# Optimization experiments

Measured on AMD Instinct MI355X. Metric: run time of the kernel, lower is better.

Reference implementation:

```python
import jax, jax.numpy as jnp
import numpy as np

L, H, NH, HD, FF, S, B, V, NL = 2, 2048, 16, 128, 4096, 1024, 2, 32000, 4
R, SCALING, BLK = 2, 16.0 / 2.0, 64  # LoRA r=2, alpha=16 -> scaling 8; NF4 blocksize 64
NF4 = jnp.array([-1.0, -0.6961928009986877, -0.5250730514526367, -0.39491748809814453,
                 -0.28444138169288635, -0.18477343022823334, -0.09105003625154495, 0.0,
                 0.07958029955625534, 0.16093020141124725, 0.24611230194568634,
                 0.33791524171829224, 0.44070982933044434, 0.5626170039176941,
                 0.7229568362236023, 1.0], dtype=jnp.float32)

def dequant(codes, scales):
    # codes [out, in] int -> NF4 values; scales [out, in//BLK] absmax per 64-block
    return NF4[codes] * jnp.repeat(scales, BLK, axis=-1)

def qlin(x, codes, scales, A, Bm):
    # fused dequant + GEMM + LoRA low-rank update: x @ (Wd + s*B@A).T
    W = dequant(codes, scales)
    return x @ W.T + SCALING * ((x @ A.T) @ Bm.T)

def layer_norm(x, g, b):
    mu = jnp.mean(x, -1, keepdims=True)
    var = jnp.var(x, -1, keepdims=True)
    return (x - mu) * jax.lax.rsqrt(var + 1e-5) * g + b

def rope(x):  # x [B,S,NH,HD]
    half = HD // 2
    inv = 1.0 / (10000.0 ** (jnp.arange(half, dtype=jnp.float32) / half))
    ang = jnp.arange(S, dtype=jnp.float32)[:, None] * inv[None, :]
    cos = jnp.concatenate([jnp.cos(ang)] * 2, -1)[None, :, None, :]
    sin = jnp.concatenate([jnp.sin(ang)] * 2, -1)[None, :, None, :]
    x1, x2 = x[..., :half], x[..., half:]
    return x * cos + jnp.concatenate([-x2, x1], -1) * sin

def setup_inputs() -> dict:
    key = jax.random.key(0)
    it = iter(jax.random.split(key, 64))
    nrm = lambda shp, s: jax.random.normal(next(it), shp, jnp.float32) * s
    cod = lambda shp: jax.random.randint(next(it), shp, 0, 16, jnp.int32)
    scl = lambda shp: jax.random.uniform(next(it), shp, jnp.float32) * 0.02 + 1e-3
    lens = jax.random.randint(next(it), (B,), S // 2, S + 1)
    return dict(
        input_ids=jax.random.randint(next(it), (B, S), 0, V, jnp.int32),
        attention_mask=(jnp.arange(S)[None, :] < lens[:, None]).astype(jnp.int32),
        labels=jax.random.randint(next(it), (B,), 0, NL, jnp.int32),
        embed=nrm((V, H), 0.02),
        qkv_codes=cod((L, 3 * H, H)), qkv_scales=scl((L, 3 * H, H // BLK)),
        qkv_A=nrm((L, R, H), 0.01), qkv_B=nrm((L, 3 * H, R), 0.01),
        dense_codes=cod((L, H, H)), dense_scales=scl((L, H, H // BLK)),
        dense_A=nrm((L, R, H), 0.01), dense_B=nrm((L, H, R), 0.01),
        min_codes=cod((L, 2 * FF, H)), min_scales=scl((L, 2 * FF, H // BLK)),
        min_A=nrm((L, R, H), 0.01), min_B=nrm((L, 2 * FF, R), 0.01),
        mout_codes=cod((L, H, FF)), mout_scales=scl((L, H, FF // BLK)),
        mout_A=nrm((L, R, FF), 0.01), mout_B=nrm((L, H, R), 0.01),
        ln1_g=jnp.ones((L, H)), ln1_b=jnp.zeros((L, H)),
        ln2_g=jnp.ones((L, H)), ln2_b=jnp.zeros((L, H)),
        lnf_g=jnp.ones((H,)), lnf_b=jnp.zeros((H,)),
        classifier_w=nrm((NL, H), 0.01),
    )

def reference(input_ids, attention_mask, labels, embed, qkv_codes, qkv_scales, qkv_A, qkv_B,
              dense_codes, dense_scales, dense_A, dense_B, min_codes, min_scales, min_A, min_B,
              mout_codes, mout_scales, mout_A, mout_B, ln1_g, ln1_b, ln2_g, ln2_b,
              lnf_g, lnf_b, classifier_w):
    x = embed[input_ids]  # [B,S,H]
    mask = jnp.tril(jnp.ones((S, S), bool))[None, None] & (attention_mask[:, None, None, :] > 0)
    for l in range(L):
        h = layer_norm(x, ln1_g[l], ln1_b[l])
        qkv = qlin(h, qkv_codes[l], qkv_scales[l], qkv_A[l], qkv_B[l]).reshape(B, S, NH, 3 * HD)
        q, k, v = qkv[..., :HD], qkv[..., HD:2 * HD], qkv[..., 2 * HD:]
        q, k = rope(q), rope(k)
        scores = jnp.einsum('bqhd,bkhd->bhqk', q, k) / np.float32(np.sqrt(HD))
        probs = jax.nn.softmax(jnp.where(mask, scores, jnp.float32(-1e30)), -1)
        attn = jnp.einsum('bhqk,bkhd->bqhd', probs, v).reshape(B, S, H)
        x = x + qlin(attn, dense_codes[l], dense_scales[l], dense_A[l], dense_B[l])
        h2 = layer_norm(x, ln2_g[l], ln2_b[l])
        u = qlin(h2, min_codes[l], min_scales[l], min_A[l], min_B[l])  # [B,S,2*FF] packed SwiGLU
        g = jax.nn.silu(u[..., :FF]) * u[..., FF:]
        x = x + qlin(g, mout_codes[l], mout_scales[l], mout_A[l], mout_B[l])
    x = layer_norm(x, lnf_g, lnf_b)
    eos = x[jnp.arange(B), attention_mask.sum(1) - 1]  # last non-padded token hidden
    logits = eos @ classifier_w.T
    logp = jax.nn.log_softmax(logits, -1)
    loss = -jnp.mean(logp[jnp.arange(B), labels])
    return loss, logits
```

## Files before the change

### kernel.cpp

```cpp
#include <hip/hip_runtime.h>

typedef unsigned short u16;
typedef __attribute__((ext_vector_type(4))) float f32x4;
typedef __attribute__((ext_vector_type(8))) short short8;
typedef __attribute__((ext_vector_type(4))) short short4v;

constexpr int CL  = 2;
constexpr int CH  = 2048;
constexpr int CNH = 16;
constexpr int CHD = 128;
constexpr int CFF = 4096;
constexpr int CS  = 1024;
constexpr int CB  = 2;
constexpr int CNL = 4;
constexpr int CM  = CB * CS;
#define SCALING 8.0f

__device__ __constant__ float NF4TAB[16] = {
    -1.0f, -0.6961928009986877f, -0.5250730514526367f, -0.39491748809814453f,
    -0.28444138169288635f, -0.18477343022823334f, -0.09105003625154495f, 0.0f,
    0.07958029955625534f, 0.16093020141124725f, 0.24611230194568634f,
    0.33791524171829224f, 0.44070982933044434f, 0.5626170039176941f,
    0.7229568362236023f, 1.0f};

__device__ __forceinline__ u16 f2bf(float f) {
  union { float f; unsigned u; } v; v.f = f;
  unsigned r = v.u + 0x7fffu + ((v.u >> 16) & 1u);
  return (u16)(r >> 16);
}
__device__ __forceinline__ float bf2f(u16 u) {
  union { unsigned u; float f; } v; v.u = ((unsigned)u) << 16;
  return v.f;
}

template <int N> __device__ __forceinline__ void wait_vm() {
  if constexpr (N == 0)      asm volatile("s_waitcnt vmcnt(0)" ::: "memory");
  else if constexpr (N == 6) asm volatile("s_waitcnt vmcnt(6)" ::: "memory");
  else if constexpr (N == 8) asm volatile("s_waitcnt vmcnt(8)" ::: "memory");
  else                       asm volatile("s_waitcnt vmcnt(0)" ::: "memory");
}

__device__ __forceinline__ float blockReduceSum(float v) {
  __shared__ float sh[4];
  #pragma unroll
  for (int o = 32; o > 0; o >>= 1) v += __shfl_down(v, o);
  __syncthreads();
  if ((threadIdx.x & 63) == 0) sh[threadIdx.x >> 6] = v;
  __syncthreads();
  return sh[0] + sh[1] + sh[2] + sh[3];
}

__global__ void k_embed(const int* __restrict__ ids, const float* __restrict__ emb,
                        float* __restrict__ x) {
  int m = blockIdx.x;
  const float4* src = (const float4*)(emb + (size_t)ids[m] * CH);
  float4* dst = (float4*)(x + (size_t)m * CH);
  for (int i = threadIdx.x; i < CH / 4; i += 256) dst[i] = src[i];
}

__global__ void k_ln_xa(const float* __restrict__ x, const float* __restrict__ g,
                        const float* __restrict__ b, const float* __restrict__ A,
                        u16* __restrict__ o, float* __restrict__ xA) {
  int m = blockIdx.x, tid = threadIdx.x;
  const float* row = x + (size_t)m * CH;
  float s = 0.f, s2 = 0.f;
  for (int i = tid; i < CH / 4; i += 256) {
    float4 v = ((const float4*)row)[i];
    s += v.x + v.y + v.z + v.w;
    s2 += v.x * v.x + v.y * v.y + v.z * v.z + v.w * v.w;
  }
  s = blockReduceSum(s);
  s2 = blockReduceSum(s2);
  float mu = s / CH, var = s2 / CH - mu * mu;
  float rs = rsqrtf(var + 1e-5f);
  u16* orow = o + (size_t)m * CH;
  float s0 = 0.f, s1 = 0.f;
  for (int i = tid; i < CH / 4; i += 256) {
    float4 v = ((const float4*)row)[i];
    float4 gv = ((const float4*)g)[i];
    float4 bv = ((const float4*)b)[i];
    float4 a0 = ((const float4*)A)[i];
    float4 a1 = ((const float4*)(A + CH))[i];
    float h0 = (v.x - mu) * rs * gv.x + bv.x;
    float h1 = (v.y - mu) * rs * gv.y + bv.y;
    float h2 = (v.z - mu) * rs * gv.z + bv.z;
    float h3 = (v.w - mu) * rs * gv.w + bv.w;
    short4v ov = { (short)f2bf(h0), (short)f2bf(h1), (short)f2bf(h2), (short)f2bf(h3) };
    *(short4v*)(orow + i * 4) = ov;
    s0 += h0 * a0.x + h1 * a0.y + h2 * a0.z + h3 * a0.w;
    s1 += h0 * a1.x + h1 * a1.y + h2 * a1.z + h3 * a1.w;
  }
  s0 = blockReduceSum(s0);
  s1 = blockReduceSum(s1);
  if (tid == 0) { xA[2 * m] = s0; xA[2 * m + 1] = s1; }
}

__global__ void k_xa(const u16* __restrict__ xb, const float* __restrict__ A,
                     float* __restrict__ xA, int K) {
  int m = blockIdx.x, tid = threadIdx.x;
  const u16* row = xb + (size_t)m * K;
  float s0 = 0.f, s1 = 0.f;
  for (int c = tid; c < K / 8; c += 256) {
    short8 v = *(const short8*)(row + c * 8);
    #pragma unroll
    for (int e = 0; e < 8; ++e) {
      float f = bf2f((u16)v[e]);
      s0 += f * A[c * 8 + e];
      s1 += f * A[K + c * 8 + e];
    }
  }
  s0 = blockReduceSum(s0);
  s1 = blockReduceSum(s1);
  if (tid == 0) { xA[2 * m] = s0; xA[2 * m + 1] = s1; }
}

__global__ void k_dequant(const int* __restrict__ codes, const float* __restrict__ scales,
                          u16* __restrict__ w, int kshift, long total) {
  __shared__ float lut[16];
  if (threadIdx.x < 16) lut[threadIdx.x] = NF4TAB[threadIdx.x];
  __syncthreads();
  long base = ((long)blockIdx.x * 256 + threadIdx.x) * 8;
  if (base >= total) return;
  long n = base >> kshift;
  int k = (int)(base & ((1L << kshift) - 1));
  float sc = scales[(size_t)n * (1 << (kshift - 6)) + (k >> 6)];
  const int* cp = codes + base;
  short8 o;
  #pragma unroll
  for (int i = 0; i < 8; ++i) o[i] = (short)f2bf(lut[cp[i] & 15] * sc);
  *(short8*)(w + base) = o;
}

__global__ void k_ropetab(float* __restrict__ cosT, float* __restrict__ sinT) {
  int i = blockIdx.x * 256 + threadIdx.x;
  if (i >= CS * 64) return;
  int s = i >> 6, d = i & 63;
  float inv = powf(10000.0f, -(float)d / 64.0f);
  float a = (float)s * inv;
  cosT[i] = cosf(a);
  sinT[i] = sinf(a);
}

__global__ void k_rope(const u16* __restrict__ qkv, const float* __restrict__ cosT,
                       const float* __restrict__ sinT, u16* __restrict__ Qb,
                       u16* __restrict__ Kb) {
  int bid = blockIdx.x;
  int s = bid & (CS - 1);
  int z = bid >> 10;
  int b = z >> 4, h = z & 15;
  int d = threadIdx.x;
  const u16* base = qkv + ((size_t)(b * CS + s)) * (3 * CH) + h * (3 * CHD);
  int dh = d & 63;
  float c = cosT[s * 64 + dh], sn = sinT[s * 64 + dh];
  float sgn = (d < 64) ? -1.0f : 1.0f;
  float q = bf2f(base[d]),       qp = bf2f(base[d ^ 64]);
  float k = bf2f(base[CHD + d]), kp = bf2f(base[CHD + (d ^ 64)]);
  size_t oi = ((size_t)z * CS + s) * CHD + d;
  Qb[oi] = f2bf(q * c + sgn * qp * sn);
  Kb[oi] = f2bf(k * c + sgn * kp * sn);
}

__global__ void k_vtrans(const u16* __restrict__ qkv, u16* __restrict__ Vt) {
  __shared__ u16 tile[32][33];
  int z = blockIdx.z;
  int b = z >> 4, h = z & 15;
  int s0 = blockIdx.x * 32, d0 = blockIdx.y * 32;
  int tx = threadIdx.x, ty = threadIdx.y;
  #pragma unroll
  for (int i = 0; i < 32; i += 8)
    tile[ty + i][tx] =
        qkv[((size_t)(b * CS + s0 + ty + i)) * (3 * CH) + h * (3 * CHD) + 2 * CHD + d0 + tx];
  __syncthreads();
  #pragma unroll
  for (int i = 0; i < 32; i += 8)
    Vt[((size_t)z * CHD + d0 + ty + i) * CS + s0 + tx] = tile[tx][ty + i];
}

__global__ __launch_bounds__(256, 2) void k_flash(
    const u16* __restrict__ Qb, const u16* __restrict__ Kb, const u16* __restrict__ Vt,
    const int* __restrict__ amask, u16* __restrict__ out) {
  __shared__ u16 Ks[64 * 128];
  __shared__ u16 Vs[128 * 64];
  __shared__ float bias[CS];
  __shared__ u16 Ps[4][16][80];
  int bid = blockIdx.x;
  int qt = 15 - (bid >> 5);
  int z = bid & 31;
  int b = z >> 4, h = z & 15;
  int tid = threadIdx.x, lane = tid & 63, wid = tid >> 6;
  int lrow = lane & 15, lgrp = lane >> 4;
  const u16* Qz = Qb + (size_t)z * CS * CHD;
  const u16* Kz = Kb + (size_t)z * CS * CHD;
  const u16* Vz = Vt + (size_t)z * CHD * CS;

  for (int i = tid; i < CS; i += 256)
    bias[i] = amask[b * CS + i] ? 0.f : -1e30f;

  int qrow = qt * 64 + wid * 16 + lrow;
  short8 qf[4];
  #pragma unroll
  for (int kk = 0; kk < 4; ++kk)
    qf[kk] = *(const short8*)(Qz + (size_t)qrow * CHD + kk * 32 + lgrp * 8);

  float m_r[4], l_r[4];
  #pragma unroll
  for (int r = 0; r < 4; ++r) { m_r[r] = -3e38f; l_r[r] = 0.f; }
  f32x4 o_acc[8];
  #pragma unroll
  for (int dj = 0; dj < 8; ++dj) o_acc[dj] = (f32x4){0.f, 0.f, 0.f, 0.f};

  const float SCL = 0.08838834764831845f;

  for (int t = 0; t <= qt; ++t) {
    int k0 = t * 64;
    __syncthreads();
    #pragma unroll
    for (int it = 0; it < 4; ++it) {
      int c = it * 256 + tid;
      int key = c >> 4, ch = c & 15;
      short8 v = *(const short8*)(Kz + (size_t)(k0 + key) * CHD + ch * 8);
      *(short8*)((char*)Ks + key * 256 + ((ch * 16) ^ ((key & 7) << 4))) = v;
    }
    #pragma unroll
    for (int it = 0; it < 4; ++it) {
      int c = it * 256 + tid;
      int d = c >> 3, ch = c & 7;
      short8 v = *(const short8*)(Vz + (size_t)d * CS + k0 + ch * 8);
      *(short8*)((char*)Vs + d * 128 + ((ch * 16) ^ ((d & 7) << 4))) = v;
    }
    __syncthreads();

    f32x4 s_acc[4];
    #pragma unroll
    for (int nj = 0; nj < 4; ++nj) s_acc[nj] = (f32x4){0.f, 0.f, 0.f, 0.f};
    #pragma unroll
    for (int kk = 0; kk < 4; ++kk) {
      #pragma unroll
      for (int nj = 0; nj < 4; ++nj) {
        int key = nj * 16 + lrow;
        short8 kf = *(const short8*)((const char*)Ks + key * 256 +
                                     (((kk * 32 + lgrp * 8) * 2) ^ ((key & 7) << 4)));
        s_acc[nj] = __builtin_amdgcn_mfma_f32_16x16x32_bf16(qf[kk], kf, s_acc[nj], 0, 0, 0);
      }
    }

    bool diag = (t == qt);
    float p[4][4], mx[4];
    #pragma unroll
    for (int r = 0; r < 4; ++r) {
      int ql = wid * 16 + 4 * lgrp + r;
      float rm = -3e38f;
      #pragma unroll
      for (int nj = 0; nj < 4; ++nj) {
        int kl = nj * 16 + lrow;
        float v = s_acc[nj][r] * SCL + bias[k0 + kl];
        if (diag && kl > ql) v = -1e30f;
        p[nj][r] = v;
        rm = fmaxf(rm, v);
      }
      mx[r] = rm;
    }
    #pragma unroll
    for (int o = 1; o < 16; o <<= 1)
      #pragma unroll
      for (int r = 0; r < 4; ++r) mx[r] = fmaxf(mx[r], __shfl_xor(mx[r], o));
    float ps[4], alpha[4];
    #pragma unroll
    for (int r = 0; r < 4; ++r) {
      float mn = fmaxf(m_r[r], mx[r]);
      alpha[r] = __expf(m_r[r] - mn);
      m_r[r] = mn;
      float acc = 0.f;
      #pragma unroll
      for (int nj = 0; nj < 4; ++nj) {
        float e = __expf(p[nj][r] - mn);
        p[nj][r] = e;
        acc += e;
      }
      ps[r] = acc;
    }
    #pragma unroll
    for (int o = 1; o < 16; o <<= 1)
      #pragma unroll
      for (int r = 0; r < 4; ++r) ps[r] += __shfl_xor(ps[r], o);
    #pragma unroll
    for (int r = 0; r < 4; ++r) {
      l_r[r] = l_r[r] * alpha[r] + ps[r];
      #pragma unroll
      for (int dj = 0; dj < 8; ++dj) o_acc[dj][r] *= alpha[r];
    }

    #pragma unroll
    for (int r = 0; r < 4; ++r)
      #pragma unroll
      for (int nj = 0; nj < 4; ++nj)
        Ps[wid][4 * lgrp + r][nj * 16 + lrow] = f2bf(p[nj][r]);
    #pragma unroll
    for (int kk2 = 0; kk2 < 2; ++kk2) {
      short8 pa = *(const short8*)(&Ps[wid][lrow][kk2 * 32 + lgrp * 8]);
      #pragma unroll
      for (int dj = 0; dj < 8; ++dj) {
        int d = dj * 16 + lrow;
        short8 vf = *(const short8*)((const char*)Vs + d * 128 +
                                     (((kk2 * 32 + lgrp * 8) * 2) ^ ((d & 7) << 4)));
        o_acc[dj] = __builtin_amdgcn_mfma_f32_16x16x32_bf16(pa, vf, o_acc[dj], 0, 0, 0);
      }
    }
  }

  #pragma unroll
  for (int r = 0; r < 4; ++r) {
    float inv = 1.0f / l_r[r];
    int qg = qt * 64 + wid * 16 + 4 * lgrp + r;
    size_t rowoff = ((size_t)(b * CS + qg)) * CH + h * CHD;
    #pragma unroll
    for (int dj = 0; dj < 8; ++dj)
      out[rowoff + dj * 16 + lrow] = f2bf(o_acc[dj][r] * inv);
  }
}

__global__ void k_silu_xa(const u16* __restrict__ u, const float* __restrict__ A,
                          u16* __restrict__ g, float* __restrict__ xA) {
  int m = blockIdx.x, tid = threadIdx.x;
  const u16* urow = u + (size_t)m * (2 * CFF);
  u16* grow = g + (size_t)m * CFF;
  float s0 = 0.f, s1 = 0.f;
  for (int c = tid; c < CFF / 8; c += 256) {
    short8 va = *(const short8*)(urow + c * 8);
    short8 vb = *(const short8*)(urow + CFF + c * 8);
    short8 og;
    #pragma unroll
    for (int e = 0; e < 8; ++e) {
      float a = bf2f((u16)va[e]);
      float bb = bf2f((u16)vb[e]);
      float gg = (a / (1.0f + __expf(-a))) * bb;
      og[e] = (short)f2bf(gg);
      s0 += gg * A[c * 8 + e];
      s1 += gg * A[CFF + c * 8 + e];
    }
    *(short8*)(grow + c * 8) = og;
  }
  s0 = blockReduceSum(s0);
  s1 = blockReduceSum(s1);
  if (tid == 0) { xA[2 * m] = s0; xA[2 * m + 1] = s1; }
}

template <int BM, int BN, int TW, int WM, int WN, int OUT_BF16, int LORA, int RESID>
__global__ __launch_bounds__(TW, 2) void k_gemm3(
    const u16* __restrict__ Ag, const u16* __restrict__ Bg, void* __restrict__ Cout,
    const float* __restrict__ resid, const float* __restrict__ xA,
    const float* __restrict__ lB, int K, int N) {
  constexpr int WROWS = BM / WM, WCOLS = BN / WN;
  constexpr int M_REP = WROWS / 16, N_REP = WCOLS / 16;
  constexpr int LA = BM * 8 / TW, LBN = BN * 8 / TW;
  constexpr int LPT = LA + LBN;
  __shared__ __align__(16) u16 As[2][BM * 64];
  __shared__ __align__(16) u16 Bs[2][BN * 64];
  int tid = threadIdx.x, lane = tid & 63, wid = tid >> 6;
  int wm = wid / WN, wn = wid % WN;
  int gx = gridDim.x, nwg = gx * gridDim.y;
  int bid = blockIdx.y * gx + blockIdx.x;
  int qq = nwg >> 3, rr = nwg & 7;
  int xcd = bid & 7, lid = bid >> 3;
  int swz = (xcd < rr ? xcd * (qq + 1) : rr * (qq + 1) + (xcd - rr) * qq) + lid;
  long bm = (long)(swz % gx) * BM, bn = (long)(swz / gx) * BN;

  f32x4 acc[M_REP][N_REP];
  #pragma unroll
  for (int i = 0; i < M_REP; ++i)
    #pragma unroll
    for (int j = 0; j < N_REP; ++j) acc[i][j] = (f32x4){0.f, 0.f, 0.f, 0.f};

  auto stage = [&](int buf, int t) {
    int k0 = t * 64;
    #pragma unroll
    for (int i = 0; i < LA; ++i) {
      int f = i * TW + tid;
      int r = f >> 3, g = (f & 7) ^ (r & 7);
      __builtin_amdgcn_global_load_lds(
          (const __attribute__((address_space(1))) void*)(Ag + (size_t)(bm + r) * K + k0 + g * 8),
          (__attribute__((address_space(3))) void*)(&As[buf][f * 8]), 16, 0, 0);
    }
    #pragma unroll
    for (int i = 0; i < LBN; ++i) {
      int f = i * TW + tid;
      int r = f >> 3, g = (f & 7) ^ (r & 7);
      __builtin_amdgcn_global_load_lds(
          (const __attribute__((address_space(1))) void*)(Bg + (size_t)(bn + r) * K + k0 + g * 8),
          (__attribute__((address_space(3))) void*)(&Bs[buf][f * 8]), 16, 0, 0);
    }
  };

  int NT = K >> 6;
  stage(0, 0);
  stage(1, 1);

  int kg = lane >> 4, lr = lane & 15;
  for (int t = 0; t < NT; ++t) {
    int buf = t & 1;
    if (t + 1 < NT) wait_vm<LPT>();
    else            wait_vm<0>();
    __builtin_amdgcn_s_barrier();

    short8 af[2][M_REP], bfr[2][N_REP];
    #pragma unroll
    for (int kk = 0; kk < 2; ++kk) {
      int au = kk * 4 + kg;
      #pragma unroll
      for (int i = 0; i < M_REP; ++i) {
        int r = wm * WROWS + i * 16 + lr;
        af[kk][i] = *(const short8*)(&As[buf][r * 64 + ((au ^ (r & 7)) << 3)]);
      }
      #pragma unroll
      for (int j = 0; j < N_REP; ++j) {
        int r = wn * WCOLS + j * 16 + lr;
        bfr[kk][j] = *(const short8*)(&Bs[buf][r * 64 + ((au ^ (r & 7)) << 3)]);
      }
    }
    asm volatile("s_waitcnt lgkmcnt(0)" ::: "memory");
    __builtin_amdgcn_s_barrier();
    if (t + 2 < NT) stage(buf, t + 2);

    __builtin_amdgcn_s_setprio(1);
    #pragma unroll
    for (int kk = 0; kk < 2; ++kk)
      #pragma unroll
      for (int i = 0; i < M_REP; ++i)
        #pragma unroll
        for (int j = 0; j < N_REP; ++j)
          acc[i][j] = __builtin_amdgcn_mfma_f32_16x16x32_bf16(af[kk][i], bfr[kk][j], acc[i][j], 0, 0, 0);
    __builtin_amdgcn_s_setprio(0);
  }

  #pragma unroll
  for (int i = 0; i < M_REP; ++i) {
    #pragma unroll
    for (int r = 0; r < 4; ++r) {
      long m = bm + wm * WROWS + i * 16 + ((lane >> 4) << 2) + r;
      float xa0 = 0.f, xa1 = 0.f;
      if (LORA) { xa0 = xA[2 * m]; xa1 = xA[2 * m + 1]; }
      #pragma unroll
      for (int j = 0; j < N_REP; ++j) {
        long n = bn + wn * WCOLS + j * 16 + (lane & 15);
        float v = acc[i][j][r];
        if (LORA) v += SCALING * (xa0 * lB[2 * n] + xa1 * lB[2 * n + 1]);
        if (RESID) v += resid[m * N + n];
        if (OUT_BF16)
          ((u16*)Cout)[m * N + n] = f2bf(v);
        else
          ((float*)Cout)[m * N + n] = v;
      }
    }
  }
}

__global__ void k_final(const float* __restrict__ x, const int* __restrict__ amask,
                        const int* __restrict__ labels, const float* __restrict__ g,
                        const float* __restrict__ bb, const float* __restrict__ cw,
                        float* __restrict__ out) {
  __shared__ float xr[CH];
  __shared__ float lg[CB][CNL];
  int tid = threadIdx.x;
  for (int b = 0; b < CB; ++b) {
    float fc = 0.f;
    for (int k = tid; k < CS; k += 256) fc += (amask[b * CS + k] != 0) ? 1.0f : 0.0f;
    int len = (int)(blockReduceSum(fc) + 0.5f);
    const float* row = x + ((size_t)b * CS + (len - 1)) * CH;
    float s = 0.f, s2 = 0.f;
    for (int k = tid; k < CH; k += 256) { float v = row[k]; s += v; s2 += v * v; }
    s = blockReduceSum(s);
    s2 = blockReduceSum(s2);
    float mu = s / CH, var = s2 / CH - mu * mu;
    float rs = rsqrtf(var + 1e-5f);
    for (int k = tid; k < CH; k += 256) xr[k] = (row[k] - mu) * rs * g[k] + bb[k];
    __syncthreads();
    for (int c = 0; c < CNL; ++c) {
      float p = 0.f;
      for (int k = tid; k < CH; k += 256) p += xr[k] * cw[c * CH + k];
      p = blockReduceSum(p);
      if (tid == 0) { lg[b][c] = p; out[1 + b * CNL + c] = p; }
    }
    __syncthreads();
  }
  if (tid == 0) {
    float loss = 0.f;
    for (int b = 0; b < CB; ++b) {
      float mx = -1e30f;
      for (int c = 0; c < CNL; ++c) mx = fmaxf(mx, lg[b][c]);
      float se = 0.f;
      for (int c = 0; c < CNL; ++c) se += expf(lg[b][c] - mx);
      float lse = mx + logf(se);
      loss -= (lg[b][labels[b]] - lse);
    }
    out[0] = loss / CB;
  }
}

static constexpr size_t X_OFF  = 0;
static constexpr size_t H_OFF  = X_OFF + (size_t)CM * CH * 4;
static constexpr size_t W_OFF  = H_OFF + (size_t)CM * CH * 2;
static constexpr size_t SC_OFF = W_OFF + (size_t)8192 * 2048 * 2;
static constexpr size_t PR_OFF = SC_OFF + (size_t)32 * CS * CS * 4;
static constexpr size_t XA_OFF = PR_OFF + (size_t)32 * CS * CS * 2;
static constexpr size_t CS_OFF = XA_OFF + (size_t)CM * 2 * 4;
static constexpr size_t SN_OFF = CS_OFF + (size_t)CS * 64 * 4;
static constexpr size_t WS_END = SN_OFF + (size_t)CS * 64 * 4;

extern "C" void kernel_launch(void* const* d_in, const int* in_sizes, int n_in,
                              void* d_out, int out_size, void* d_ws, size_t ws_size,
                              hipStream_t stream) {
  (void)in_sizes; (void)n_in; (void)out_size;
  if (ws_size < WS_END) return;

  const int*   ids          = (const int*)d_in[0];
  const int*   amask        = (const int*)d_in[1];
  const int*   labels       = (const int*)d_in[2];
  const float* emb          = (const float*)d_in[3];
  const int*   qkv_codes    = (const int*)d_in[4];
  const float* qkv_scales   = (const float*)d_in[5];
  const float* qkv_A        = (const float*)d_in[6];
  const float* qkv_B        = (const float*)d_in[7];
  const int*   dense_codes  = (const int*)d_in[8];
  const float* dense_scales = (const float*)d_in[9];
  const float* dense_A      = (const float*)d_in[10];
  const float* dense_B      = (const float*)d_in[11];
  const int*   min_codes    = (const int*)d_in[12];
  const float* min_scales   = (const float*)d_in[13];
  const float* min_A        = (const float*)d_in[14];
  const float* min_B        = (const float*)d_in[15];
  const int*   mout_codes   = (const int*)d_in[16];
  const float* mout_scales  = (const float*)d_in[17];
  const float* mout_A       = (const float*)d_in[18];
  const float* mout_B       = (const float*)d_in[19];
  const float* ln1_g        = (const float*)d_in[20];
  const float* ln1_b        = (const float*)d_in[21];
  const float* ln2_g        = (const float*)d_in[22];
  const float* ln2_b        = (const float*)d_in[23];
  const float* lnf_g        = (const float*)d_in[24];
  const float* lnf_b        = (const float*)d_in[25];
  const float* cw           = (const float*)d_in[26];

  char* ws = (char*)d_ws;
  float* x       = (float*)(ws + X_OFF);
  u16*   hbuf    = (u16*)(ws + H_OFF);
  u16*   wbuf    = (u16*)(ws + W_OFF);
  u16*   Qb      = (u16*)(ws + W_OFF);
  u16*   Kb      = (u16*)(ws + W_OFF + (size_t)32 * CS * CHD * 2);
  u16*   Vt      = (u16*)(ws + W_OFF + (size_t)64 * CS * CHD * 2);
  u16*   qkv_out = (u16*)(ws + SC_OFF);
  u16*   ubuf    = (u16*)(ws + SC_OFF);
  u16*   gbuf    = (u16*)(ws + PR_OFF);
  float* xA      = (float*)(ws + XA_OFF);
  float* cosT    = (float*)(ws + CS_OFF);
  float* sinT    = (float*)(ws + SN_OFF);

  k_ropetab<<<(CS * 64 + 255) / 256, 256, 0, stream>>>(cosT, sinT);
  k_embed<<<CM, 256, 0, stream>>>(ids, emb, x);

  for (int l = 0; l < CL; ++l) {
    k_ln_xa<<<CM, 256, 0, stream>>>(x, ln1_g + l * CH, ln1_b + l * CH,
                                    qkv_A + (size_t)l * 2 * CH, hbuf, xA);
    long nq = (long)3 * CH * CH;
    k_dequant<<<(int)(nq / 8 / 256), 256, 0, stream>>>(
        qkv_codes + (size_t)l * nq, qkv_scales + (size_t)l * 3 * CH * (CH / 64),
        wbuf, 11, nq);
    k_gemm3<128, 128, 256, 2, 2, 1, 1, 0><<<dim3(CM / 128, (3 * CH) / 128), 256, 0, stream>>>(
        hbuf, wbuf, qkv_out, nullptr, xA, qkv_B + (size_t)l * 3 * CH * 2, CH, 3 * CH);
    k_rope<<<32 * CS, 128, 0, stream>>>(qkv_out, cosT, sinT, Qb, Kb);
    k_vtrans<<<dim3(CS / 32, CHD / 32, 32), dim3(32, 8), 0, stream>>>(qkv_out, Vt);
    k_flash<<<512, 256, 0, stream>>>(Qb, Kb, Vt, amask, hbuf);
    k_xa<<<CM, 256, 0, stream>>>(hbuf, dense_A + (size_t)l * 2 * CH, xA, CH);
    long nd = (long)CH * CH;
    k_dequant<<<(int)(nd / 8 / 256), 256, 0, stream>>>(
        dense_codes + (size_t)l * nd, dense_scales + (size_t)l * CH * (CH / 64),
        wbuf, 11, nd);
    k_gemm3<128, 64, 256, 2, 2, 0, 1, 1><<<dim3(CM / 128, CH / 64), 256, 0, stream>>>(
        hbuf, wbuf, x, x, xA, dense_B + (size_t)l * CH * 2, CH, CH);

    k_ln_xa<<<CM, 256, 0, stream>>>(x, ln2_g + l * CH, ln2_b + l * CH,
                                    min_A + (size_t)l * 2 * CH, hbuf, xA);
    long nm = (long)2 * CFF * CH;
    k_dequant<<<(int)(nm / 8 / 256), 256, 0, stream>>>(
        min_codes + (size_t)l * nm, min_scales + (size_t)l * 2 * CFF * (CH / 64),
        wbuf, 11, nm);
    k_gemm3<128, 128, 256, 2, 2, 1, 1, 0><<<dim3(CM / 128, (2 * CFF) / 128), 256, 0, stream>>>(
        hbuf, wbuf, ubuf, nullptr, xA, min_B + (size_t)l * 2 * CFF * 2, CH, 2 * CFF);
    k_silu_xa<<<CM, 256, 0, stream>>>(ubuf, mout_A + (size_t)l * 2 * CFF, gbuf, xA);
    long no = (long)CH * CFF;
    k_dequant<<<(int)(no / 8 / 256), 256, 0, stream>>>(
        mout_codes + (size_t)l * no, mout_scales + (size_t)l * CH * (CFF / 64),
        wbuf, 12, no);
    k_gemm3<128, 64, 256, 2, 2, 0, 1, 1><<<dim3(CM / 128, CH / 64), 256, 0, stream>>>(
        gbuf, wbuf, x, x, xA, mout_B + (size_t)l * CH * 2, CFF, CH);
  }

  k_final<<<1, 256, 0, stream>>>(x, amask, labels, lnf_g, lnf_b, cw, (float*)d_out);
}
```

Before: 735.1 us.

## Add 256x256 eight-wave GEMM with direct-to-LDS loads for QKV and MLP-in

Introduces a new GEMM kernel with 256x256 tiles and 8 waves. It loads global data directly into LDS using a swizzled layout and double buffering, and interleaves loads, fragment reads and MFMA quarters behind barriers with priority hints. It also remaps blocks across XCDs. The kernel replaces the earlier 128x128 GEMM for the two wide projections, aiming to raise data reuse and overlap memory with compute. The cost is a large LDS footprint, high register pressure and a fragile hand-written wait-count schedule.

```diff
diff --git a/kernel.cpp b/kernel.cpp
--- a/kernel.cpp
+++ b/kernel.cpp
@@ -449,6 +449,138 @@
           ((u16*)Cout)[m * N + n] = f2bf(v);
         else
           ((float*)Cout)[m * N + n] = v;
+      }
+    }
+  }
+}
+
+#define RD_A(d, mh)                                                              \
+  { _Pragma("unroll") for (int kk = 0; kk < 2; ++kk) {                           \
+      _Pragma("unroll") for (int ii = 0; ii < 4; ++ii) {                         \
+        int ra = ((mh) * 4 + ii) * 16 + lr;                                      \
+        int slot = (kk * 4 + kg) ^ ((lr >> 1) & 3);                              \
+        a_f[kk][ii] = *(const short8*)(&As[d][wm][ra * 64 + slot * 8]);          \
+      } } }
+#define RD_B(d, nh)                                                              \
+  { _Pragma("unroll") for (int kk = 0; kk < 2; ++kk) {                           \
+      _Pragma("unroll") for (int jj = 0; jj < 2; ++jj) {                         \
+        int rb = (wn & 1) * 64 + ((nh) * 2 + jj) * 16 + lr;                      \
+        int slot = (kk * 4 + kg) ^ ((lr >> 1) & 3);                              \
+        b_f[nh][kk][jj] = *(const short8*)(&Bs[d][wn >> 1][rb * 64 + slot * 8]); \
+      } } }
+#define MFMA_Q(mh, nh)                                                           \
+  { __builtin_amdgcn_s_setprio(1);                                               \
+    _Pragma("unroll") for (int kk = 0; kk < 2; ++kk) {                           \
+      _Pragma("unroll") for (int ii = 0; ii < 4; ++ii) {                         \
+        _Pragma("unroll") for (int jj = 0; jj < 2; ++jj) {                       \
+          acc[(mh) * 4 + ii][(nh) * 2 + jj] =                                    \
+              __builtin_amdgcn_mfma_f32_16x16x32_bf16(                           \
+                  a_f[kk][ii], b_f[nh][kk][jj],                                  \
+                  acc[(mh) * 4 + ii][(nh) * 2 + jj], 0, 0, 0);                   \
+        } } }                                                                    \
+    __builtin_amdgcn_s_setprio(0); }
+#define LGKM0_SB                                                                 \
+  asm volatile("s_waitcnt lgkmcnt(0)" ::: "memory");                             \
+  __builtin_amdgcn_sched_barrier(0);
+#define BAR __builtin_amdgcn_s_barrier();
+
+__global__ __launch_bounds__(512, 2) void k_gemm8(
+    const u16* __restrict__ Ag, const u16* __restrict__ Bg, u16* __restrict__ Cout,
+    const float* __restrict__ xA, const float* __restrict__ lB, int K, int N) {
+  __shared__ __align__(16) u16 As[2][2][128 * 64];
+  __shared__ __align__(16) u16 Bs[2][2][128 * 64];
+  int tid = threadIdx.x, lane = tid & 63, wid = tid >> 6;
+  int wm = wid >> 2, wn = wid & 3;
+  int kg = lane >> 4, lr = lane & 15;
+  int gx = gridDim.x, nwg = gx * gridDim.y;
+  int bid = blockIdx.y * gx + blockIdx.x;
+  int qq = nwg >> 3, rr = nwg & 7;
+  int xcd = bid & 7, lid = bid >> 3;
+  int swz = (xcd < rr ? xcd * (qq + 1) : rr * (qq + 1) + (xcd - rr) * qq) + lid;
+  long bm = (long)(swz % gx) * 256, bn = (long)(swz / gx) * 256;
+  const int NKT = K >> 6;
+
+  f32x4 acc[8][4];
+  #pragma unroll
+  for (int i = 0; i < 8; ++i)
+    #pragma unroll
+    for (int j = 0; j < 4; ++j) acc[i][j] = (f32x4){0.f, 0.f, 0.f, 0.f};
+  short8 a_f[2][4], b_f[2][2][2];
+
+  auto stA = [&](int t, int h) {
+    int d = t & 1;
+    int tt = t < NKT ? t : NKT - 1;
+    int k0 = tt << 6;
+    #pragma unroll
+    for (int ld = 0; ld < 2; ++ld) {
+      int f = ld * 512 + tid;
+      int row = f >> 3, p = f & 7;
+      int ss = p ^ ((row >> 1) & 3);
+      __builtin_amdgcn_global_load_lds(
+          (const __attribute__((address_space(1))) void*)(Ag + (size_t)(bm + h * 128 + row) * K + k0 + ss * 8),
+          (__attribute__((address_space(3))) void*)(&As[d][h][f * 8]), 16, 0, 0);
+    }
+  };
+  auto stB = [&](int t, int h) {
+    int d = t & 1;
+    int tt = t < NKT ? t : NKT - 1;
+    int k0 = tt << 6;
+    #pragma unroll
+    for (int ld = 0; ld < 2; ++ld) {
+      int f = ld * 512 + tid;
+      int row = f >> 3, p = f & 7;
+      int ss = p ^ ((row >> 1) & 3);
+      __builtin_amdgcn_global_load_lds(
+          (const __attribute__((address_space(1))) void*)(Bg + (size_t)(bn + h * 128 + row) * K + k0 + ss * 8),
+          (__attribute__((address_space(3))) void*)(&Bs[d][h][f * 8]), 16, 0, 0);
+    }
+  };
+
+  stA(0, 0); stA(0, 1); stB(0, 0); stB(0, 1);
+  stB(1, 0); stA(1, 0);
+  asm volatile("s_waitcnt vmcnt(4)" ::: "memory");
+  BAR
+
+  int NI = NKT >> 1;
+  for (int j = 0; j < NI; ++j) {
+    int t0 = 2 * j;
+    RD_A(0, 0) RD_B(0, 0)
+    stA(t0 + 1, 1);
+    BAR LGKM0_SB MFMA_Q(0, 0) BAR
+    RD_B(0, 1)
+    stB(t0 + 1, 1);
+    BAR LGKM0_SB MFMA_Q(0, 1) BAR
+    RD_A(0, 1)
+    stB(t0 + 2, 0);
+    BAR LGKM0_SB MFMA_Q(1, 0) BAR
+    stA(t0 + 2, 0);
+    asm volatile("s_waitcnt vmcnt(2)" ::: "memory");
+    BAR MFMA_Q(1, 1) BAR
+    RD_A(1, 0) RD_B(1, 0)
+    stA(t0 + 2, 1);
+    BAR LGKM0_SB MFMA_Q(0, 0) BAR
+    RD_B(1, 1)
+    stB(t0 + 2, 1);
+    BAR LGKM0_SB MFMA_Q(0, 1) BAR
+    RD_A(1, 1)
+    stB(t0 + 3, 0);
+    BAR LGKM0_SB MFMA_Q(1, 0) BAR
+    stA(t0 + 3, 0);
+    asm volatile("s_waitcnt vmcnt(2)" ::: "memory");
+    BAR MFMA_Q(1, 1) BAR
+  }
+
+  #pragma unroll
+  for (int i = 0; i < 8; ++i) {
+    #pragma unroll
+    for (int r = 0; r < 4; ++r) {
+      long m = bm + wm * 128 + i * 16 + ((lane >> 4) << 2) + r;
+      float xa0 = xA[2 * m], xa1 = xA[2 * m + 1];
+      #pragma unroll
+      for (int j = 0; j < 4; ++j) {
+        long n = bn + wn * 64 + j * 16 + (lane & 15);
+        float v = acc[i][j][r] + SCALING * (xa0 * lB[2 * n] + xa1 * lB[2 * n + 1]);
+        Cout[m * N + n] = f2bf(v);
       }
     }
   }
@@ -564,8 +696,8 @@
     k_dequant<<<(int)(nq / 8 / 256), 256, 0, stream>>>(
         qkv_codes + (size_t)l * nq, qkv_scales + (size_t)l * 3 * CH * (CH / 64),
         wbuf, 11, nq);
-    k_gemm3<128, 128, 256, 2, 2, 1, 1, 0><<<dim3(CM / 128, (3 * CH) / 128), 256, 0, stream>>>(
-        hbuf, wbuf, qkv_out, nullptr, xA, qkv_B + (size_t)l * 3 * CH * 2, CH, 3 * CH);
+    k_gemm8<<<dim3(CM / 256, (3 * CH) / 256), 512, 0, stream>>>(
+        hbuf, wbuf, qkv_out, xA, qkv_B + (size_t)l * 3 * CH * 2, CH, 3 * CH);
     k_rope<<<32 * CS, 128, 0, stream>>>(qkv_out, cosT, sinT, Qb, Kb);
     k_vtrans<<<dim3(CS / 32, CHD / 32, 32), dim3(32, 8), 0, stream>>>(qkv_out, Vt);
     k_flash<<<512, 256, 0, stream>>>(Qb, Kb, Vt, amask, hbuf);
@@ -583,8 +715,8 @@
     k_dequant<<<(int)(nm / 8 / 256), 256, 0, stream>>>(
         min_codes + (size_t)l * nm, min_scales + (size_t)l * 2 * CFF * (CH / 64),
         wbuf, 11, nm);
-    k_gemm3<128, 128, 256, 2, 2, 1, 1, 0><<<dim3(CM / 128, (2 * CFF) / 128), 256, 0, stream>>>(
-        hbuf, wbuf, ubuf, nullptr, xA, min_B + (size_t)l * 2 * CFF * 2, CH, 2 * CFF);
+    k_gemm8<<<dim3(CM / 256, (2 * CFF) / 256), 512, 0, stream>>>(
+        hbuf, wbuf, ubuf, xA, min_B + (size_t)l * 2 * CFF * 2, CH, 2 * CFF);
     k_silu_xa<<<CM, 256, 0, stream>>>(ubuf, mout_A + (size_t)l * 2 * CFF, gbuf, xA);
     long no = (long)CH * CFF;
     k_dequant<<<(int)(no / 8 / 256), 256, 0, stream>>>(
```

After: 775.1 us. 1.05x slower.

## Pair causal query tiles per block and double-buffer K/V via async LDS loads

Applied to the files above, without the earlier changes.

The flash attention kernel now gives each block two query tiles (p and 15-p) so every block does the same amount of causal work, and launches 256 blocks instead of 512. K and V tiles are double-buffered in LDS using global_load_lds async copies with manual vmcnt waits and barriers, so the next tile's loads overlap the current tile's MFMA and softmax work. This roughly doubles LDS use and register pressure (two sets of accumulators, launch bounds lowered to one block per CU). The hand-tuned waitcnt counts are a correctness risk.

```diff
diff --git a/kernel.cpp b/kernel.cpp
--- a/kernel.cpp
+++ b/kernel.cpp
@@ -176,146 +176,175 @@
     Vt[((size_t)z * CHD + d0 + ty + i) * CS + s0 + tx] = tile[tx][ty + i];
 }
 
-__global__ __launch_bounds__(256, 2) void k_flash(
+#define FLASH_TILE(S, T, QT, QF, MR, LR, OA)                                     \
+  {                                                                              \
+    int k0_ = (T) * 64;                                                          \
+    const u16* KsT = Ks[S][(T) & 1];                                             \
+    const u16* VsT = Vs[S][(T) & 1];                                             \
+    f32x4 s_acc[4];                                                              \
+    _Pragma("unroll") for (int nj = 0; nj < 4; ++nj)                             \
+        s_acc[nj] = (f32x4){0.f, 0.f, 0.f, 0.f};                                 \
+    _Pragma("unroll") for (int kk = 0; kk < 4; ++kk) {                           \
+      _Pragma("unroll") for (int nj = 0; nj < 4; ++nj) {                         \
+        int key = nj * 16 + lrow;                                                \
+        int slot = (kk * 4 + lgrp) ^ (key & 7);                                  \
+        short8 kf = *(const short8*)(KsT + key * 128 + slot * 8);                \
+        s_acc[nj] = __builtin_amdgcn_mfma_f32_16x16x32_bf16(QF[kk], kf,          \
+                                                            s_acc[nj], 0, 0, 0); \
+      } }                                                                        \
+    bool diag = ((T) == (QT));                                                   \
+    float pp[4][4], mx[4];                                                       \
+    _Pragma("unroll") for (int r = 0; r < 4; ++r) {                              \
+      int ql = wid * 16 + 4 * lgrp + r;                                          \
+      float rm = -3e38f;                                                         \
+      _Pragma("unroll") for (int nj = 0; nj < 4; ++nj) {                         \
+        int kl = nj * 16 + lrow;                                                 \
+        float v = s_acc[nj][r] * SCL + bias[k0_ + kl];                           \
+        if (diag && kl > ql) v = -1e30f;                                         \
+        pp[nj][r] = v;                                                           \
+        rm = fmaxf(rm, v);                                                       \
+      }                                                                          \
+      mx[r] = rm;                                                                \
+    }                                                                            \
+    _Pragma("unroll") for (int o = 1; o < 16; o <<= 1)                           \
+      _Pragma("unroll") for (int r = 0; r < 4; ++r)                              \
+        mx[r] = fmaxf(mx[r], __shfl_xor(mx[r], o));                              \
+    float psum[4], alpha[4];                                                     \
+    _Pragma("unroll") for (int r = 0; r < 4; ++r) {                              \
+      float mn = fmaxf(MR[r], mx[r]);                                            \
+      alpha[r] = __expf(MR[r] - mn);                                             \
+      MR[r] = mn;                                                                \
+      float a2 = 0.f;                                                            \
+      _Pragma("unroll") for (int nj = 0; nj < 4; ++nj) {                         \
+        float e = __expf(pp[nj][r] - mn);                                        \
+        pp[nj][r] = e;                                                           \
+        a2 += e;                                                                 \
+      }                                                                          \
+      psum[r] = a2;                                                              \
+    }                                                                            \
+    _Pragma("unroll") for (int o = 1; o < 16; o <<= 1)                           \
+      _Pragma("unroll") for (int r = 0; r < 4; ++r)                              \
+        psum[r] += __shfl_xor(psum[r], o);                                       \
+    _Pragma("unroll") for (int r = 0; r < 4; ++r) {                              \
+      LR[r] = LR[r] * alpha[r] + psum[r];                                        \
+      _Pragma("unroll") for (int dj = 0; dj < 8; ++dj) OA[dj][r] *= alpha[r];    \
+    }                                                                            \
+    _Pragma("unroll") for (int r = 0; r < 4; ++r)                                \
+      _Pragma("unroll") for (int nj = 0; nj < 4; ++nj)                           \
+        Ps[wid][4 * lgrp + r][nj * 16 + lrow] = f2bf(pp[nj][r]);                 \
+    _Pragma("unroll") for (int kk2 = 0; kk2 < 2; ++kk2) {                        \
+      short8 pa = *(const short8*)(&Ps[wid][lrow][kk2 * 32 + lgrp * 8]);         \
+      _Pragma("unroll") for (int dj = 0; dj < 8; ++dj) {                         \
+        int d = dj * 16 + lrow;                                                  \
+        int slot = (kk2 * 4 + lgrp) ^ (d & 7);                                   \
+        short8 vf = *(const short8*)(VsT + d * 64 + slot * 8);                   \
+        OA[dj] = __builtin_amdgcn_mfma_f32_16x16x32_bf16(pa, vf, OA[dj],         \
+                                                         0, 0, 0);               \
+      } }                                                                        \
+  }
+
+__global__ __launch_bounds__(256, 1) void k_flash3(
     const u16* __restrict__ Qb, const u16* __restrict__ Kb, const u16* __restrict__ Vt,
     const int* __restrict__ amask, u16* __restrict__ out) {
-  __shared__ u16 Ks[64 * 128];
-  __shared__ u16 Vs[128 * 64];
+  __shared__ __align__(16) u16 Ks[2][2][64 * 128];
+  __shared__ __align__(16) u16 Vs[2][2][128 * 64];
   __shared__ float bias[CS];
   __shared__ u16 Ps[4][16][80];
   int bid = blockIdx.x;
-  int qt = 15 - (bid >> 5);
-  int z = bid & 31;
+  int z = bid & 31, p = bid >> 5;
+  int qtA = p, qtB = 15 - p;
+  int NTA = qtA + 1, NTB = qtB + 1;
   int b = z >> 4, h = z & 15;
   int tid = threadIdx.x, lane = tid & 63, wid = tid >> 6;
   int lrow = lane & 15, lgrp = lane >> 4;
   const u16* Qz = Qb + (size_t)z * CS * CHD;
   const u16* Kz = Kb + (size_t)z * CS * CHD;
   const u16* Vz = Vt + (size_t)z * CHD * CS;
+  const float SCL = 0.08838834764831845f;
 
   for (int i = tid; i < CS; i += 256)
     bias[i] = amask[b * CS + i] ? 0.f : -1e30f;
 
-  int qrow = qt * 64 + wid * 16 + lrow;
-  short8 qf[4];
-  #pragma unroll
-  for (int kk = 0; kk < 4; ++kk)
-    qf[kk] = *(const short8*)(Qz + (size_t)qrow * CHD + kk * 32 + lgrp * 8);
-
-  float m_r[4], l_r[4];
-  #pragma unroll
-  for (int r = 0; r < 4; ++r) { m_r[r] = -3e38f; l_r[r] = 0.f; }
-  f32x4 o_acc[8];
-  #pragma unroll
-  for (int dj = 0; dj < 8; ++dj) o_acc[dj] = (f32x4){0.f, 0.f, 0.f, 0.f};
-
-  const float SCL = 0.08838834764831845f;
-
-  for (int t = 0; t <= qt; ++t) {
-    int k0 = t * 64;
-    __syncthreads();
-    #pragma unroll
-    for (int it = 0; it < 4; ++it) {
-      int c = it * 256 + tid;
-      int key = c >> 4, ch = c & 15;
-      short8 v = *(const short8*)(Kz + (size_t)(k0 + key) * CHD + ch * 8);
-      *(short8*)((char*)Ks + key * 256 + ((ch * 16) ^ ((key & 7) << 4))) = v;
-    }
-    #pragma unroll
-    for (int it = 0; it < 4; ++it) {
-      int c = it * 256 + tid;
-      int d = c >> 3, ch = c & 7;
-      short8 v = *(const short8*)(Vz + (size_t)d * CS + k0 + ch * 8);
-      *(short8*)((char*)Vs + d * 128 + ((ch * 16) ^ ((d & 7) << 4))) = v;
-    }
-    __syncthreads();
-
-    f32x4 s_acc[4];
-    #pragma unroll
-    for (int nj = 0; nj < 4; ++nj) s_acc[nj] = (f32x4){0.f, 0.f, 0.f, 0.f};
-    #pragma unroll
-    for (int kk = 0; kk < 4; ++kk) {
-      #pragma unroll
-      for (int nj = 0; nj < 4; ++nj) {
-        int key = nj * 16 + lrow;
-        short8 kf = *(const short8*)((const char*)Ks + key * 256 +
-                                     (((kk * 32 + lgrp * 8) * 2) ^ ((key & 7) << 4)));
-        s_acc[nj] = __builtin_amdgcn_mfma_f32_16x16x32_bf16(qf[kk], kf, s_acc[nj], 0, 0, 0);
-      }
-    }
-
-    bool diag = (t == qt);
-    float p[4][4], mx[4];
-    #pragma unroll
-    for (int r = 0; r < 4; ++r) {
-      int ql = wid * 16 + 4 * lgrp + r;
-      float rm = -3e38f;
-      #pragma unroll
-      for (int nj = 0; nj < 4; ++nj) {
-        int kl = nj * 16 + lrow;
-        float v = s_acc[nj][r] * SCL + bias[k0 + kl];
-        if (diag && kl > ql) v = -1e30f;
-        p[nj][r] = v;
-        rm = fmaxf(rm, v);
-      }
-      mx[r] = rm;
-    }
-    #pragma unroll
-    for (int o = 1; o < 16; o <<= 1)
-      #pragma unroll
-      for (int r = 0; r < 4; ++r) mx[r] = fmaxf(mx[r], __shfl_xor(mx[r], o));
-    float ps[4], alpha[4];
-    #pragma unroll
-    for (int r = 0; r < 4; ++r) {
-      float mn = fmaxf(m_r[r], mx[r]);
-      alpha[r] = __expf(m_r[r] - mn);
-      m_r[r] = mn;
-      float acc = 0.f;
-      #pragma unroll
-      for (int nj = 0; nj < 4; ++nj) {
-        float e = __expf(p[nj][r] - mn);
-        p[nj][r] = e;
-        acc += e;
-      }
-      ps[r] = acc;
-    }
-    #pragma unroll
-    for (int o = 1; o < 16; o <<= 1)
-      #pragma unroll
-      for (int r = 0; r < 4; ++r) ps[r] += __shfl_xor(ps[r], o);
-    #pragma unroll
-    for (int r = 0; r < 4; ++r) {
-      l_r[r] = l_r[r] * alpha[r] + ps[r];
-      #pragma unroll
-      for (int dj = 0; dj < 8; ++dj) o_acc[dj][r] *= alpha[r];
-    }
-
-    #pragma unroll
-    for (int r = 0; r < 4; ++r)
-      #pragma unroll
-      for (int nj = 0; nj < 4; ++nj)
-        Ps[wid][4 * lgrp + r][nj * 16 + lrow] = f2bf(p[nj][r]);
-    #pragma unroll
-    for (int kk2 = 0; kk2 < 2; ++kk2) {
-      short8 pa = *(const short8*)(&Ps[wid][lrow][kk2 * 32 + lgrp * 8]);
-      #pragma unroll
-      for (int dj = 0; dj < 8; ++dj) {
-        int d = dj * 16 + lrow;
-        short8 vf = *(const short8*)((const char*)Vs + d * 128 +
-                                     (((kk2 * 32 + lgrp * 8) * 2) ^ ((d & 7) << 4)));
-        o_acc[dj] = __builtin_amdgcn_mfma_f32_16x16x32_bf16(pa, vf, o_acc[dj], 0, 0, 0);
-      }
-    }
+  short8 qfA[4], qfB[4];
+  int qrA = qtA * 64 + wid * 16 + lrow;
+  int qrB = qtB * 64 + wid * 16 + lrow;
+  #pragma unroll
+  for (int kk = 0; kk < 4; ++kk) {
+    qfA[kk] = *(const short8*)(Qz + (size_t)qrA * CHD + kk * 32 + lgrp * 8);
+    qfB[kk] = *(const short8*)(Qz + (size_t)qrB * CHD + kk * 32 + lgrp * 8);
+  }
+  asm volatile("s_waitcnt lgkmcnt(0)" ::: "memory");
+
+  float mA[4], lA[4], mB[4], lB[4];
+  f32x4 oA[8], oB[8];
+  #pragma unroll
+  for (int r = 0; r < 4; ++r) { mA[r] = -3e38f; lA[r] = 0.f; mB[r] = -3e38f; lB[r] = 0.f; }
+  #pragma unroll
+  for (int dj = 0; dj < 8; ++dj) {
+    oA[dj] = (f32x4){0.f, 0.f, 0.f, 0.f};
+    oB[dj] = (f32x4){0.f, 0.f, 0.f, 0.f};
+  }
+
+  auto stage = [&](int s, int t, int NT) {
+    int tt = t < NT ? t : NT - 1;
+    int k0 = tt << 6, d = t & 1;
+    #pragma unroll
+    for (int ld = 0; ld < 4; ++ld) {
+      int f = ld * 256 + tid;
+      int r = f >> 4, g = (f & 15) ^ (r & 7);
+      __builtin_amdgcn_global_load_lds(
+          (const __attribute__((address_space(1))) void*)(Kz + (size_t)(k0 + r) * CHD + g * 8),
+          (__attribute__((address_space(3))) void*)(&Ks[s][d][f * 8]), 16, 0, 0);
+    }
+    #pragma unroll
+    for (int ld = 0; ld < 4; ++ld) {
+      int f = ld * 256 + tid;
+      int r = f >> 3, g = (f & 7) ^ (r & 7);
+      __builtin_amdgcn_global_load_lds(
+          (const __attribute__((address_space(1))) void*)(Vz + (size_t)r * CS + k0 + g * 8),
+          (__attribute__((address_space(3))) void*)(&Vs[s][d][f * 8]), 16, 0, 0);
+    }
+  };
+
+  stage(0, 0, NTA); stage(1, 0, NTB);
+  stage(0, 1, NTA); stage(1, 1, NTB);
+
+  for (int t = 0; t < NTA; ++t) {
+    asm volatile("s_waitcnt vmcnt(24)" ::: "memory");
+    __builtin_amdgcn_s_barrier();
+    FLASH_TILE(0, t, qtA, qfA, mA, lA, oA)
+    asm volatile("s_waitcnt lgkmcnt(0)" ::: "memory");
+    __builtin_amdgcn_s_barrier();
+    stage(0, t + 2, NTA);
+    asm volatile("s_waitcnt vmcnt(24)" ::: "memory");
+    __builtin_amdgcn_s_barrier();
+    FLASH_TILE(1, t, qtB, qfB, mB, lB, oB)
+    asm volatile("s_waitcnt lgkmcnt(0)" ::: "memory");
+    __builtin_amdgcn_s_barrier();
+    stage(1, t + 2, NTB);
+  }
+  for (int t = NTA; t < NTB; ++t) {
+    asm volatile("s_waitcnt vmcnt(8)" ::: "memory");
+    __builtin_amdgcn_s_barrier();
+    FLASH_TILE(1, t, qtB, qfB, mB, lB, oB)
+    asm volatile("s_waitcnt lgkmcnt(0)" ::: "memory");
+    __builtin_amdgcn_s_barrier();
+    stage(1, t + 2, NTB);
   }
 
   #pragma unroll
   for (int r = 0; r < 4; ++r) {
-    float inv = 1.0f / l_r[r];
-    int qg = qt * 64 + wid * 16 + 4 * lgrp + r;
-    size_t rowoff = ((size_t)(b * CS + qg)) * CH + h * CHD;
-    #pragma unroll
-    for (int dj = 0; dj < 8; ++dj)
-      out[rowoff + dj * 16 + lrow] = f2bf(o_acc[dj][r] * inv);
+    float invA = 1.0f / lA[r];
+    int qgA = qtA * 64 + wid * 16 + 4 * lgrp + r;
+    size_t roA = ((size_t)(b * CS + qgA)) * CH + h * CHD;
+    float invB = 1.0f / lB[r];
+    int qgB = qtB * 64 + wid * 16 + 4 * lgrp + r;
+    size_t roB = ((size_t)(b * CS + qgB)) * CH + h * CHD;
+    #pragma unroll
+    for (int dj = 0; dj < 8; ++dj) {
+      out[roA + dj * 16 + lrow] = f2bf(oA[dj][r] * invA);
+      out[roB + dj * 16 + lrow] = f2bf(oB[dj][r] * invB);
+    }
   }
 }
 
@@ -568,7 +597,7 @@
         hbuf, wbuf, qkv_out, nullptr, xA, qkv_B + (size_t)l * 3 * CH * 2, CH, 3 * CH);
     k_rope<<<32 * CS, 128, 0, stream>>>(qkv_out, cosT, sinT, Qb, Kb);
     k_vtrans<<<dim3(CS / 32, CHD / 32, 32), dim3(32, 8), 0, stream>>>(qkv_out, Vt);
-    k_flash<<<512, 256, 0, stream>>>(Qb, Kb, Vt, amask, hbuf);
+    k_flash3<<<256, 256, 0, stream>>>(Qb, Kb, Vt, amask, hbuf);
     k_xa<<<CM, 256, 0, stream>>>(hbuf, dense_A + (size_t)l * 2 * CH, xA, CH);
     long nd = (long)CH * CH;
     k_dequant<<<(int)(nd / 8 / 256), 256, 0, stream>>>(
```

Measured after the change: 754.4 us. 2.6% more time.
